# Kernel tuning notes

Hardware: AMD Instinct MI355X
Metric: run time of the kernel (lower is better)

The kernel has to match this reference:

```python
import jax, jax.numpy as jnp
import numpy as np

HEADERS = 8
LN_EPS = 1e-3  # keras LayerNormalization default


def setup_inputs() -> dict:
    key = jax.random.key(0)
    ks = jax.random.split(key, 8)
    B, H, W, C = 16, 48, 160, 512
    shi = C // HEADERS
    scale = 1.0 / np.sqrt(C)
    return {
        "x": jax.random.normal(ks[0], (B, H, W, C), dtype=jnp.float32),
        "w_mask": jax.random.normal(ks[1], (shi,), dtype=jnp.float32) * (1.0 / np.sqrt(shi)),
        "b_mask": jnp.zeros((1,), dtype=jnp.float32),
        "w1": jax.random.normal(ks[2], (C, C), dtype=jnp.float32) * scale,
        "b1": jnp.zeros((C,), dtype=jnp.float32),
        "gamma": jnp.ones((C,), dtype=jnp.float32),
        "beta": jnp.zeros((C,), dtype=jnp.float32),
        "w2": jax.random.normal(ks[3], (C, C), dtype=jnp.float32) * scale,
        "b2": jnp.zeros((C,), dtype=jnp.float32),
    }


def reference(x, w_mask, b_mask, w1, b1, gamma, beta, w2, b2):
    B, H, W, C = x.shape
    g = HEADERS
    shi = C // g
    # split channels into headers: [B, g, H*W, shi]
    xh = x.reshape(B, H, W, g, shi).transpose(0, 3, 1, 2, 4).reshape(B, g, H * W, shi)
    # 1x1 conv to single channel -> attention logits over spatial positions
    logits = jnp.einsum('bgnc,c->bgn', xh, w_mask) + b_mask[0]
    # att_scale=True and headers>1 -> rescale
    logits = logits / jnp.sqrt(jnp.asarray(shi, x.dtype))
    attn = jax.nn.softmax(logits, axis=-1)  # softmax over H*W
    # single-query attention pooling per header -> [B, g, shi] -> [B, C]
    ctx = jnp.einsum('bgnc,bgn->bgc', xh, attn).reshape(B, C)
    # transform: 1x1 conv -> LayerNorm over C -> ReLU -> 1x1 conv
    h = ctx @ w1 + b1
    mu = jnp.mean(h, axis=-1, keepdims=True)
    var = jnp.mean(jnp.square(h - mu), axis=-1, keepdims=True)
    hn = (h - mu) * jax.lax.rsqrt(var + LN_EPS) * gamma + beta
    t = jax.nn.relu(hn) @ w2 + b2  # [B, C]
    return x + t[:, None, None, :]
```

## Files before the change

kernel.cpp:

```cpp
#include <hip/hip_runtime.h>
#include <math.h>

#define Bb 16
#define Hh 48
#define Ww 160
#define Cc 512
#define Gg 8
#define SHI 64
#define Nn (Hh * Ww)
#define NCH 64
#define POSCH (Nn / NCH)
#define LN_EPS 1e-3f

typedef float v4f __attribute__((ext_vector_type(4)));

__device__ __forceinline__ float wave_sum(float v) {
#pragma unroll
    for (int o = 32; o > 0; o >>= 1) v += __shfl_xor(v, o);
    return v;
}
__device__ __forceinline__ float wave_max(float v) {
#pragma unroll
    for (int o = 32; o > 0; o >>= 1) v = fmaxf(v, __shfl_xor(v, o));
    return v;
}

__global__ __launch_bounds__(256) void k_pool(const float* __restrict__ x,
                                              const float* __restrict__ w_mask,
                                              const float* __restrict__ b_mask,
                                              float* __restrict__ pctx,
                                              float* __restrict__ pms) {
    int chunk = blockIdx.x;
    int b = blockIdx.y;
    int t = threadIdx.x;
    int w = t >> 6;
    int lane = t & 63;
    int g = lane >> 3;

    int cw = (lane & 7) * 8;
    float4 m0 = *(const float4*)(w_mask + cw);
    float4 m1 = *(const float4*)(w_mask + cw + 4);
    float bm = b_mask[0];

    float mrun = -1e30f, srun = 0.f;
    float acc[8];
#pragma unroll
    for (int j = 0; j < 8; ++j) acc[j] = 0.f;

    const float* xbase = x + ((size_t)b * Nn + (size_t)chunk * POSCH) * Cc + lane * 8;

    for (int p = w; p < POSCH; p += 4) {
        const float* xp = xbase + (size_t)p * Cc;
        float4 a0 = *(const float4*)(xp);
        float4 a1 = *(const float4*)(xp + 4);
        float v[8] = {a0.x, a0.y, a0.z, a0.w, a1.x, a1.y, a1.z, a1.w};
        float d = a0.x * m0.x + a0.y * m0.y + a0.z * m0.z + a0.w * m0.w
                + a1.x * m1.x + a1.y * m1.y + a1.z * m1.z + a1.w * m1.w;
        d += __shfl_xor(d, 1);
        d += __shfl_xor(d, 2);
        d += __shfl_xor(d, 4);
        float l = (d + bm) * 0.125f;
        float mnew = fmaxf(mrun, l);
        float scale = __expf(mrun - mnew);
        float e = __expf(l - mnew);
        srun = srun * scale + e;
#pragma unroll
        for (int j = 0; j < 8; ++j) acc[j] = acc[j] * scale + e * v[j];
        mrun = mnew;
    }

    __shared__ float lm[4][8], lsv[4][8];
    __shared__ float lacc[4][Cc];
    if ((lane & 7) == 0) { lm[w][g] = mrun; lsv[w][g] = srun; }
    __syncthreads();
    float M = fmaxf(fmaxf(lm[0][g], lm[1][g]), fmaxf(lm[2][g], lm[3][g]));
    float wscale = __expf(mrun - M);
#pragma unroll
    for (int j = 0; j < 8; ++j) lacc[w][lane * 8 + j] = acc[j] * wscale;
    __syncthreads();
    for (int c = t; c < Cc; c += 256) {
        float s4 = lacc[0][c] + lacc[1][c] + lacc[2][c] + lacc[3][c];
        pctx[((size_t)b * NCH + chunk) * Cc + c] = s4;
    }
    if (t < 8) {
        int gg = t;
        float Mg = fmaxf(fmaxf(lm[0][gg], lm[1][gg]), fmaxf(lm[2][gg], lm[3][gg]));
        float Sg = lsv[0][gg] * __expf(lm[0][gg] - Mg) + lsv[1][gg] * __expf(lm[1][gg] - Mg)
                 + lsv[2][gg] * __expf(lm[2][gg] - Mg) + lsv[3][gg] * __expf(lm[3][gg] - Mg);
        pms[(((size_t)b * Gg + gg) * NCH + chunk) * 2 + 0] = Mg;
        pms[(((size_t)b * Gg + gg) * NCH + chunk) * 2 + 1] = Sg;
    }
}

__global__ __launch_bounds__(512) void k_mlp(const float* __restrict__ pctx,
                                             const float* __restrict__ pms,
                                             const float* __restrict__ w1,
                                             const float* __restrict__ b1,
                                             const float* __restrict__ gamma,
                                             const float* __restrict__ beta,
                                             const float* __restrict__ w2,
                                             const float* __restrict__ b2,
                                             float* __restrict__ tvec) {
    int b = blockIdx.x;
    int t = threadIdx.x;
    int lane = t & 63, wid = t >> 6;
    __shared__ float escale[Gg][NCH];
    __shared__ float Sg[Gg];
    __shared__ float cs[Cc];
    __shared__ float hs[Cc];
    __shared__ float red[8];

    {
        int g = wid, ch = lane;
        float2 msv = *(const float2*)(pms + (((size_t)b * Gg + g) * NCH + ch) * 2);
        float M = wave_max(msv.x);
        float e = __expf(msv.x - M);
        escale[g][ch] = e;
        float S = wave_sum(msv.y * e);
        if (lane == 0) Sg[g] = S;
    }
    __syncthreads();

    {
        int g = t >> 6;
        float invS = 1.0f / Sg[g];
        float a = 0.f;
#pragma unroll 4
        for (int ch = 0; ch < NCH; ++ch)
            a += pctx[((size_t)b * NCH + ch) * Cc + t] * escale[g][ch];
        cs[t] = a * invS;
    }
    __syncthreads();

    float h = b1[t];
#pragma unroll 8
    for (int k = 0; k < Cc; ++k) h = fmaf(cs[k], w1[(size_t)k * Cc + t], h);

    float s = wave_sum(h);
    if (lane == 0) red[wid] = s;
    __syncthreads();
    float mu = 0.f;
#pragma unroll
    for (int k = 0; k < 8; ++k) mu += red[k];
    mu *= (1.0f / Cc);
    __syncthreads();
    float d = h - mu;
    float sq = wave_sum(d * d);
    if (lane == 0) red[wid] = sq;
    __syncthreads();
    float var = 0.f;
#pragma unroll
    for (int k = 0; k < 8; ++k) var += red[k];
    var *= (1.0f / Cc);
    float hn = d * rsqrtf(var + LN_EPS) * gamma[t] + beta[t];
    hs[t] = fmaxf(hn, 0.f);
    __syncthreads();

    float tv = b2[t];
#pragma unroll 8
    for (int k = 0; k < Cc; ++k) tv = fmaf(hs[k], w2[(size_t)k * Cc + t], tv);
    tvec[(size_t)b * Cc + t] = tv;
}

__global__ __launch_bounds__(256) void k_resid(const v4f* __restrict__ x4,
                                               const v4f* __restrict__ t4,
                                               v4f* __restrict__ o4) {
    int b = blockIdx.y;
    int idx = (blockIdx.x * 256 + threadIdx.x) * 2;
    int c4a = idx & 127;
    size_t off = (size_t)b * (Nn * (Cc / 4)) + idx;
    v4f xv0 = __builtin_nontemporal_load(&x4[off]);
    v4f xv1 = __builtin_nontemporal_load(&x4[off + 1]);
    v4f tv0 = t4[b * (Cc / 4) + c4a];
    v4f tv1 = t4[b * (Cc / 4) + c4a + 1];
    v4f o0 = xv0 + tv0;
    v4f o1 = xv1 + tv1;
    __builtin_nontemporal_store(o0, &o4[off]);
    __builtin_nontemporal_store(o1, &o4[off + 1]);
}

extern "C" void kernel_launch(void* const* d_in, const int* in_sizes, int n_in,
                              void* d_out, int out_size, void* d_ws, size_t ws_size,
                              hipStream_t stream) {
    const float* x      = (const float*)d_in[0];
    const float* w_mask = (const float*)d_in[1];
    const float* b_mask = (const float*)d_in[2];
    const float* w1     = (const float*)d_in[3];
    const float* b1     = (const float*)d_in[4];
    const float* gamma  = (const float*)d_in[5];
    const float* beta   = (const float*)d_in[6];
    const float* w2     = (const float*)d_in[7];
    const float* b2     = (const float*)d_in[8];
    float* out = (float*)d_out;

    float* ws   = (float*)d_ws;
    float* pctx = ws;
    float* pms  = pctx + (size_t)Bb * NCH * Cc;
    float* tvec = pms + (size_t)Bb * Gg * NCH * 2;

    k_pool<<<dim3(NCH, Bb), 256, 0, stream>>>(x, w_mask, b_mask, pctx, pms);
    k_mlp<<<Bb, Cc, 0, stream>>>(pctx, pms, w1, b1, gamma, beta, w2, b2, tvec);
    k_resid<<<dim3((Nn * Cc / 4) / 512, Bb), 256, 0, stream>>>(
        (const v4f*)x, (const v4f*)tvec, (v4f*)out);
}
```

Before: 536.8 us.

## Fuse pool, MLP and residual into one cooperative kernel with grid syncs

Merges the three kernels into one cooperative launch of 64x16 blocks. Grid-wide barriers separate the pooling phase, a per-batch MLP run by one block per batch, and the residual add. Each block then adds t to the same x chunk it pooled, hoping to reuse cache and save launch gaps. The cost is that 1008 blocks sit idle during the serial MLP phase, there are two grid syncs, and all 1024 blocks must be co-resident for the cooperative launch to work.

```diff
diff --git a/kernel.cpp b/kernel.cpp
--- a/kernel.cpp
+++ b/kernel.cpp
@@ -1,13 +1,13 @@
 #include <hip/hip_runtime.h>
+#include <hip/hip_cooperative_groups.h>
 #include <math.h>
 
+namespace cg = cooperative_groups;
+
 #define Bb 16
-#define Hh 48
-#define Ww 160
 #define Cc 512
 #define Gg 8
-#define SHI 64
-#define Nn (Hh * Ww)
+#define Nn 7680
 #define NCH 64
 #define POSCH (Nn / NCH)
 #define LN_EPS 1e-3f
@@ -25,158 +25,165 @@
     return v;
 }
 
-__global__ __launch_bounds__(256) void k_pool(const float* __restrict__ x,
-                                              const float* __restrict__ w_mask,
-                                              const float* __restrict__ b_mask,
-                                              float* __restrict__ pctx,
-                                              float* __restrict__ pms) {
-    int chunk = blockIdx.x;
-    int b = blockIdx.y;
-    int t = threadIdx.x;
-    int w = t >> 6;
-    int lane = t & 63;
-    int g = lane >> 3;
-
-    int cw = (lane & 7) * 8;
-    float4 m0 = *(const float4*)(w_mask + cw);
-    float4 m1 = *(const float4*)(w_mask + cw + 4);
-    float bm = b_mask[0];
-
-    float mrun = -1e30f, srun = 0.f;
-    float acc[8];
-#pragma unroll
-    for (int j = 0; j < 8; ++j) acc[j] = 0.f;
-
-    const float* xbase = x + ((size_t)b * Nn + (size_t)chunk * POSCH) * Cc + lane * 8;
-
-    for (int p = w; p < POSCH; p += 4) {
-        const float* xp = xbase + (size_t)p * Cc;
-        float4 a0 = *(const float4*)(xp);
-        float4 a1 = *(const float4*)(xp + 4);
-        float v[8] = {a0.x, a0.y, a0.z, a0.w, a1.x, a1.y, a1.z, a1.w};
-        float d = a0.x * m0.x + a0.y * m0.y + a0.z * m0.z + a0.w * m0.w
-                + a1.x * m1.x + a1.y * m1.y + a1.z * m1.z + a1.w * m1.w;
-        d += __shfl_xor(d, 1);
-        d += __shfl_xor(d, 2);
-        d += __shfl_xor(d, 4);
-        float l = (d + bm) * 0.125f;
-        float mnew = fmaxf(mrun, l);
-        float scale = __expf(mrun - mnew);
-        float e = __expf(l - mnew);
-        srun = srun * scale + e;
-#pragma unroll
-        for (int j = 0; j < 8; ++j) acc[j] = acc[j] * scale + e * v[j];
-        mrun = mnew;
-    }
+__global__ __launch_bounds__(256) void k_fused(
+    const float* __restrict__ x, const float* __restrict__ w_mask,
+    const float* __restrict__ b_mask, const float* __restrict__ w1,
+    const float* __restrict__ b1, const float* __restrict__ gamma,
+    const float* __restrict__ beta, const float* __restrict__ w2,
+    const float* __restrict__ b2, float* __restrict__ pctx,
+    float* __restrict__ pms, float* __restrict__ tvec,
+    float* __restrict__ out)
+{
+    cg::grid_group grid = cg::this_grid();
+    const int chunk = blockIdx.x;
+    const int b = blockIdx.y;
+    const int t = threadIdx.x;
+    const int w = t >> 6;
+    const int lane = t & 63;
+    const int g = lane >> 3;
 
     __shared__ float lm[4][8], lsv[4][8];
     __shared__ float lacc[4][Cc];
-    if ((lane & 7) == 0) { lm[w][g] = mrun; lsv[w][g] = srun; }
-    __syncthreads();
-    float M = fmaxf(fmaxf(lm[0][g], lm[1][g]), fmaxf(lm[2][g], lm[3][g]));
-    float wscale = __expf(mrun - M);
-#pragma unroll
-    for (int j = 0; j < 8; ++j) lacc[w][lane * 8 + j] = acc[j] * wscale;
-    __syncthreads();
-    for (int c = t; c < Cc; c += 256) {
-        float s4 = lacc[0][c] + lacc[1][c] + lacc[2][c] + lacc[3][c];
-        pctx[((size_t)b * NCH + chunk) * Cc + c] = s4;
-    }
-    if (t < 8) {
-        int gg = t;
-        float Mg = fmaxf(fmaxf(lm[0][gg], lm[1][gg]), fmaxf(lm[2][gg], lm[3][gg]));
-        float Sg = lsv[0][gg] * __expf(lm[0][gg] - Mg) + lsv[1][gg] * __expf(lm[1][gg] - Mg)
-                 + lsv[2][gg] * __expf(lm[2][gg] - Mg) + lsv[3][gg] * __expf(lm[3][gg] - Mg);
-        pms[(((size_t)b * Gg + gg) * NCH + chunk) * 2 + 0] = Mg;
-        pms[(((size_t)b * Gg + gg) * NCH + chunk) * 2 + 1] = Sg;
-    }
-}
-
-__global__ __launch_bounds__(512) void k_mlp(const float* __restrict__ pctx,
-                                             const float* __restrict__ pms,
-                                             const float* __restrict__ w1,
-                                             const float* __restrict__ b1,
-                                             const float* __restrict__ gamma,
-                                             const float* __restrict__ beta,
-                                             const float* __restrict__ w2,
-                                             const float* __restrict__ b2,
-                                             float* __restrict__ tvec) {
-    int b = blockIdx.x;
-    int t = threadIdx.x;
-    int lane = t & 63, wid = t >> 6;
     __shared__ float escale[Gg][NCH];
-    __shared__ float Sg[Gg];
+    __shared__ float SgS[Gg];
     __shared__ float cs[Cc];
     __shared__ float hs[Cc];
-    __shared__ float red[8];
+    __shared__ float red[4];
+    __shared__ float tl[Cc];
 
     {
-        int g = wid, ch = lane;
-        float2 msv = *(const float2*)(pms + (((size_t)b * Gg + g) * NCH + ch) * 2);
-        float M = wave_max(msv.x);
-        float e = __expf(msv.x - M);
-        escale[g][ch] = e;
-        float S = wave_sum(msv.y * e);
-        if (lane == 0) Sg[g] = S;
+        int cw = (lane & 7) * 8;
+        float4 m0 = *(const float4*)(w_mask + cw);
+        float4 m1 = *(const float4*)(w_mask + cw + 4);
+        float bm = b_mask[0];
+
+        float mrun = -1e30f, srun = 0.f;
+        float acc[8];
+#pragma unroll
+        for (int j = 0; j < 8; ++j) acc[j] = 0.f;
+
+        const float* xbase = x + ((size_t)b * Nn + (size_t)chunk * POSCH) * Cc + lane * 8;
+        for (int p = w; p < POSCH; p += 4) {
+            const float* xp = xbase + (size_t)p * Cc;
+            float4 a0 = *(const float4*)(xp);
+            float4 a1 = *(const float4*)(xp + 4);
+            float v[8] = {a0.x, a0.y, a0.z, a0.w, a1.x, a1.y, a1.z, a1.w};
+            float d = a0.x * m0.x + a0.y * m0.y + a0.z * m0.z + a0.w * m0.w
+                    + a1.x * m1.x + a1.y * m1.y + a1.z * m1.z + a1.w * m1.w;
+            d += __shfl_xor(d, 1);
+            d += __shfl_xor(d, 2);
+            d += __shfl_xor(d, 4);
+            float l = (d + bm) * 0.125f;
+            float mnew = fmaxf(mrun, l);
+            float scale = __expf(mrun - mnew);
+            float e = __expf(l - mnew);
+            srun = srun * scale + e;
+#pragma unroll
+            for (int j = 0; j < 8; ++j) acc[j] = acc[j] * scale + e * v[j];
+            mrun = mnew;
+        }
+
+        if ((lane & 7) == 0) { lm[w][g] = mrun; lsv[w][g] = srun; }
+        __syncthreads();
+        float M = fmaxf(fmaxf(lm[0][g], lm[1][g]), fmaxf(lm[2][g], lm[3][g]));
+        float wscale = __expf(mrun - M);
+#pragma unroll
+        for (int j = 0; j < 8; ++j) lacc[w][lane * 8 + j] = acc[j] * wscale;
+        __syncthreads();
+        for (int c = t; c < Cc; c += 256) {
+            float s4 = lacc[0][c] + lacc[1][c] + lacc[2][c] + lacc[3][c];
+            pctx[((size_t)b * NCH + chunk) * Cc + c] = s4;
+        }
+        if (t < 8) {
+            int gg = t;
+            float Mg = fmaxf(fmaxf(lm[0][gg], lm[1][gg]), fmaxf(lm[2][gg], lm[3][gg]));
+            float Sg = lsv[0][gg] * __expf(lm[0][gg] - Mg) + lsv[1][gg] * __expf(lm[1][gg] - Mg)
+                     + lsv[2][gg] * __expf(lm[2][gg] - Mg) + lsv[3][gg] * __expf(lm[3][gg] - Mg);
+            pms[(((size_t)b * Gg + gg) * NCH + chunk) * 2 + 0] = Mg;
+            pms[(((size_t)b * Gg + gg) * NCH + chunk) * 2 + 1] = Sg;
+        }
     }
+
+    grid.sync();
+
+    if (chunk == 0) {
+        for (int gi = 2 * w; gi <= 2 * w + 1; ++gi) {
+            float2 msv = *(const float2*)(pms + (((size_t)b * Gg + gi) * NCH + lane) * 2);
+            float M = wave_max(msv.x);
+            float e = __expf(msv.x - M);
+            escale[gi][lane] = e;
+            float S = wave_sum(msv.y * e);
+            if (lane == 0) SgS[gi] = S;
+        }
+        __syncthreads();
+        {
+            int g0 = t >> 6, g1 = (t + 256) >> 6;
+            float a0 = 0.f, a1 = 0.f;
+#pragma unroll 4
+            for (int ch = 0; ch < NCH; ++ch) {
+                const float* p = pctx + ((size_t)b * NCH + ch) * Cc;
+                a0 += p[t] * escale[g0][ch];
+                a1 += p[t + 256] * escale[g1][ch];
+            }
+            cs[t] = a0 / SgS[g0];
+            cs[t + 256] = a1 / SgS[g1];
+        }
+        __syncthreads();
+
+        float h0 = b1[t], h1 = b1[t + 256];
+#pragma unroll 8
+        for (int k = 0; k < Cc; ++k) {
+            float c = cs[k];
+            const float* r = w1 + (size_t)k * Cc;
+            h0 = fmaf(c, r[t], h0);
+            h1 = fmaf(c, r[t + 256], h1);
+        }
+
+        float s = wave_sum(h0 + h1);
+        if (lane == 0) red[w] = s;
+        __syncthreads();
+        float mu = (red[0] + red[1] + red[2] + red[3]) * (1.0f / Cc);
+        __syncthreads();
+        float d0 = h0 - mu, d1 = h1 - mu;
+        float sq = wave_sum(d0 * d0 + d1 * d1);
+        if (lane == 0) red[w] = sq;
+        __syncthreads();
+        float var = (red[0] + red[1] + red[2] + red[3]) * (1.0f / Cc);
+        float rs = rsqrtf(var + LN_EPS);
+        hs[t]       = fmaxf(d0 * rs * gamma[t] + beta[t], 0.f);
+        hs[t + 256] = fmaxf(d1 * rs * gamma[t + 256] + beta[t + 256], 0.f);
+        __syncthreads();
+
+        float tv0 = b2[t], tv1 = b2[t + 256];
+#pragma unroll 8
+        for (int k = 0; k < Cc; ++k) {
+            float hh = hs[k];
+            const float* r = w2 + (size_t)k * Cc;
+            tv0 = fmaf(hh, r[t], tv0);
+            tv1 = fmaf(hh, r[t + 256], tv1);
+        }
+        tvec[(size_t)b * Cc + t] = tv0;
+        tvec[(size_t)b * Cc + t + 256] = tv1;
+    }
+
+    grid.sync();
+
+    tl[t] = tvec[(size_t)b * Cc + t];
+    tl[t + 256] = tvec[(size_t)b * Cc + t + 256];
     __syncthreads();
-
     {
-        int g = t >> 6;
-        float invS = 1.0f / Sg[g];
-        float a = 0.f;
-#pragma unroll 4
-        for (int ch = 0; ch < NCH; ++ch)
-            a += pctx[((size_t)b * NCH + ch) * Cc + t] * escale[g][ch];
-        cs[t] = a * invS;
+        const size_t base = ((size_t)b * Nn + (size_t)chunk * POSCH) * Cc;
+        const v4f* x4 = (const v4f*)(x + base);
+        v4f* o4 = (v4f*)(out + base);
+        const int total4 = POSCH * (Cc / 4);
+        for (int i = t; i < total4; i += 256) {
+            int c4 = i & 127;
+            v4f xv = x4[i];
+            v4f tv = *(const v4f*)(&tl[c4 * 4]);
+            v4f ov = xv + tv;
+            __builtin_nontemporal_store(ov, &o4[i]);
+        }
     }
-    __syncthreads();
-
-    float h = b1[t];
-#pragma unroll 8
-    for (int k = 0; k < Cc; ++k) h = fmaf(cs[k], w1[(size_t)k * Cc + t], h);
-
-    float s = wave_sum(h);
-    if (lane == 0) red[wid] = s;
-    __syncthreads();
-    float mu = 0.f;
-#pragma unroll
-    for (int k = 0; k < 8; ++k) mu += red[k];
-    mu *= (1.0f / Cc);
-    __syncthreads();
-    float d = h - mu;
-    float sq = wave_sum(d * d);
-    if (lane == 0) red[wid] = sq;
-    __syncthreads();
-    float var = 0.f;
-#pragma unroll
-    for (int k = 0; k < 8; ++k) var += red[k];
-    var *= (1.0f / Cc);
-    float hn = d * rsqrtf(var + LN_EPS) * gamma[t] + beta[t];
-    hs[t] = fmaxf(hn, 0.f);
-    __syncthreads();
-
-    float tv = b2[t];
-#pragma unroll 8
-    for (int k = 0; k < Cc; ++k) tv = fmaf(hs[k], w2[(size_t)k * Cc + t], tv);
-    tvec[(size_t)b * Cc + t] = tv;
-}
-
-__global__ __launch_bounds__(256) void k_resid(const v4f* __restrict__ x4,
-                                               const v4f* __restrict__ t4,
-                                               v4f* __restrict__ o4) {
-    int b = blockIdx.y;
-    int idx = (blockIdx.x * 256 + threadIdx.x) * 2;
-    int c4a = idx & 127;
-    size_t off = (size_t)b * (Nn * (Cc / 4)) + idx;
-    v4f xv0 = __builtin_nontemporal_load(&x4[off]);
-    v4f xv1 = __builtin_nontemporal_load(&x4[off + 1]);
-    v4f tv0 = t4[b * (Cc / 4) + c4a];
-    v4f tv1 = t4[b * (Cc / 4) + c4a + 1];
-    v4f o0 = xv0 + tv0;
-    v4f o1 = xv1 + tv1;
-    __builtin_nontemporal_store(o0, &o4[off]);
-    __builtin_nontemporal_store(o1, &o4[off + 1]);
 }
 
 extern "C" void kernel_launch(void* const* d_in, const int* in_sizes, int n_in,
@@ -198,8 +205,10 @@
     float* pms  = pctx + (size_t)Bb * NCH * Cc;
     float* tvec = pms + (size_t)Bb * Gg * NCH * 2;
 
-    k_pool<<<dim3(NCH, Bb), 256, 0, stream>>>(x, w_mask, b_mask, pctx, pms);
-    k_mlp<<<Bb, Cc, 0, stream>>>(pctx, pms, w1, b1, gamma, beta, w2, b2, tvec);
-    k_resid<<<dim3((Nn * Cc / 4) / 512, Bb), 256, 0, stream>>>(
-        (const v4f*)x, (const v4f*)tvec, (v4f*)out);
-}
+    void* args[] = { (void*)&x, (void*)&w_mask, (void*)&b_mask, (void*)&w1,
+                     (void*)&b1, (void*)&gamma, (void*)&beta, (void*)&w2,
+                     (void*)&b2, (void*)&pctx, (void*)&pms, (void*)&tvec,
+                     (void*)&out };
+    hipLaunchCooperativeKernel((const void*)k_fused, dim3(NCH, Bb),
+                               dim3(256, 1, 1), args, 0, stream);
+}
```

Measured after the change: 774.0 us. +44.2%, slower.
